# Kernel optimization log

Measured on AMD Instinct MI355X. Metric: run time of the kernel, lower is better.

Reference implementation:

```python
import jax, jax.numpy as jnp
import numpy as np

HEADS = 8
DIM_HEAD = 160
QUERY_DIM = 1280
INNER = HEADS * DIM_HEAD  # 1280
B, S = 2, 4096


def setup_inputs() -> dict:
    key = jax.random.key(0)
    ks = jax.random.split(key, 7)
    scale = 0.02
    return {
        "hidden_states": jax.random.normal(ks[0], (B, QUERY_DIM, 1, S), jnp.float32),
        "context": jax.random.normal(ks[1], (B, QUERY_DIM, 1, S), jnp.float32),
        "mask": jnp.zeros((B, S, 1, 1), jnp.float32),
        "Wq": jax.random.normal(ks[2], (INNER, QUERY_DIM), jnp.float32) * scale,
        "Wk": jax.random.normal(ks[3], (INNER, QUERY_DIM), jnp.float32) * scale,
        "Wv": jax.random.normal(ks[4], (INNER, QUERY_DIM), jnp.float32) * scale,
        "Wout": jax.random.normal(ks[5], (QUERY_DIM, INNER), jnp.float32) * scale,
        "bout": jnp.zeros((QUERY_DIM,), jnp.float32),
    }


def reference(hidden_states, context, mask, Wq, Wk, Wv, Wout, bout):
    # hidden_states/context: [B, C, 1, S]; 1x1 conv == channel-dim matmul.
    x = hidden_states[:, :, 0, :]  # [B, C, Sq]
    c = context[:, :, 0, :]        # [B, C, Sk]
    scale = DIM_HEAD ** (-0.5)

    q = jnp.einsum("oc,bcs->bos", Wq, x)  # [B, inner, Sq]
    k = jnp.einsum("oc,bcs->bos", Wk, c)  # [B, inner, Sk]
    v = jnp.einsum("oc,bcs->bos", Wv, c)  # [B, inner, Sk]

    bsz, _, sq = q.shape
    sk = k.shape[-1]
    qh = q.reshape(bsz, HEADS, DIM_HEAD, sq)
    kh = k.reshape(bsz, HEADS, DIM_HEAD, sk)
    vh = v.reshape(bsz, HEADS, DIM_HEAD, sk)

    # split_einsum: per-head q^T k * scale, mask added per kv position,
    # softmax over kv dim. Vectorized over heads here (same math).
    scores = jnp.einsum("bhdq,bhdk->bhqk", qh, kh) * scale  # [B,H,Sq,Sk]
    scores = scores + mask[:, 0:, 0, 0][:, None, None, :]   # mask over kv
    weights = jax.nn.softmax(scores, axis=-1)
    attn = jnp.einsum("bhqk,bhdk->bhdq", weights, vh)       # [B,H,Dh,Sq]
    attn = attn.reshape(bsz, INNER, sq)

    out = jnp.einsum("oc,bcs->bos", Wout, attn) + bout[None, :, None]
    return out[:, :, None, :]  # [B, C, 1, Sq]
```

## Files before the change

kernel.cpp:

```cpp
#include <hip/hip_runtime.h>
#include <hip/hip_bf16.h>
#include <math.h>

#define B_   2
#define S_   4096
#define H_   8
#define D_   160
#define QD_  1280
#define SCALE 0.07905694150420949f
#define LOG2E 1.4426950408889634f

typedef unsigned short ushort_t;
typedef __attribute__((ext_vector_type(8))) short short8;
typedef __attribute__((ext_vector_type(4))) float f32x4;

#define MFMA16(a, b, c) __builtin_amdgcn_mfma_f32_16x16x32_bf16(a, b, c, 0, 0, 0)

__device__ __forceinline__ ushort_t f2bf(float f) {
  unsigned u = __float_as_uint(f);
  u += 0x7fffu + ((u >> 16) & 1u);
  return (ushort_t)(u >> 16);
}
__device__ __forceinline__ ushort_t f2bf_fast(float f) {
  return (ushort_t)((__float_as_uint(f) + 0x8000u) >> 16);
}

__device__ __forceinline__ void gload_lds16(const ushort_t* g, ushort_t* l) {
  __builtin_amdgcn_global_load_lds(
      (const __attribute__((address_space(1))) unsigned int*)(g),
      (__attribute__((address_space(3))) unsigned int*)(l), 16, 0, 0);
}

template <int CTRL>
__device__ __forceinline__ float dpp_mov(float x) {
  return __int_as_float(
      __builtin_amdgcn_update_dpp(0, __float_as_int(x), CTRL, 0xF, 0xF, true));
}
__device__ __forceinline__ float row_sum16(float x) {
  x += dpp_mov<0xB1>(x);
  x += dpp_mov<0x4E>(x);
  x += dpp_mov<0x124>(x);
  x += dpp_mov<0x128>(x);
  return x;
}

__global__ __launch_bounds__(256) void transpose_cvt(
    const float* __restrict__ src, ushort_t* __restrict__ dst)
{
  const int b = blockIdx.z;
  const int s0 = blockIdx.x * 32;
  const int c0 = blockIdx.y * 32;
  __shared__ float T[32][33];
  const int t = threadIdx.x;
  const int sl = t & 31, cr = t >> 5;
#pragma unroll
  for (int i = 0; i < 4; ++i)
    T[cr + i * 8][sl] = src[((size_t)b * QD_ + c0 + cr + i * 8) * S_ + s0 + sl];
  __syncthreads();
  const int cl = (t & 7) * 4, sr = t >> 3;
  ushort4 v;
  v.x = f2bf(T[cl + 0][sr]);
  v.y = f2bf(T[cl + 1][sr]);
  v.z = f2bf(T[cl + 2][sr]);
  v.w = f2bf(T[cl + 3][sr]);
  *(ushort4*)(dst + ((size_t)b * S_ + s0 + sr) * QD_ + c0 + cl) = v;
}

__global__ __launch_bounds__(256) void cvt_w(
    const float* __restrict__ w0, const float* __restrict__ w1,
    const float* __restrict__ w2, const float* __restrict__ w3,
    ushort_t* __restrict__ o0, ushort_t* __restrict__ o1,
    ushort_t* __restrict__ o2, ushort_t* __restrict__ o3)
{
  const int which = blockIdx.y;
  const float* s = which == 0 ? w0 : which == 1 ? w1 : which == 2 ? w2 : w3;
  ushort_t* d    = which == 0 ? o0 : which == 1 ? o1 : which == 2 ? o2 : o3;
  const size_t i = ((size_t)blockIdx.x * 256 + threadIdx.x) * 4;
  const float4 f = *(const float4*)(s + i);
  ushort4 v;
  v.x = f2bf(f.x); v.y = f2bf(f.y); v.z = f2bf(f.z); v.w = f2bf(f.w);
  *(ushort4*)(d + i) = v;
}

#define GBM 128
#define GBN 128
#define GBK 32

__global__ __launch_bounds__(256) void gemm_mfma(
    const ushort_t* __restrict__ A, const ushort_t* __restrict__ B,
    void* __restrict__ Cp, const float* __restrict__ bias,
    int M, int N, int K, int mode,
    size_t strideA, size_t strideB, size_t strideC)
{
  const int bz = blockIdx.z;
  const int m0 = blockIdx.y * GBM;
  const int n0 = blockIdx.x * GBN;
  const ushort_t* __restrict__ Ab = A + (size_t)bz * strideA;
  const ushort_t* __restrict__ Bb = B + (size_t)bz * strideB;

  __shared__ ushort_t As[GBM * GBK];
  __shared__ ushort_t Bs[GBN * GBK];

  const int t = threadIdx.x;
  const int wid = t >> 6, lane = t & 63;
  const int l16 = lane & 15, quad = lane >> 4;
  const int wm = (wid >> 1) * 64, wn = (wid & 1) * 64;

  f32x4 acc[4][4];
#pragma unroll
  for (int i = 0; i < 4; ++i)
#pragma unroll
    for (int j = 0; j < 4; ++j) acc[i][j] = {0.f, 0.f, 0.f, 0.f};

  for (int k0 = 0; k0 < K; k0 += GBK) {
    __syncthreads();
#pragma unroll
    for (int i = 0; i < 2; ++i) {
      const int G = (i * 4 + wid) * 64 + lane;
      const int r = G >> 2, sl = G & 3;
      const int g = sl ^ (r & 3);
      gload_lds16(Ab + (size_t)(m0 + r) * K + k0 + g * 8, &As[(i * 4 + wid) * 512]);
      gload_lds16(Bb + (size_t)(n0 + r) * K + k0 + g * 8, &Bs[(i * 4 + wid) * 512]);
    }
    __syncthreads();

    short8 af[4], bfr[4];
#pragma unroll
    for (int mt = 0; mt < 4; ++mt) {
      const int r = wm + mt * 16 + l16;
      af[mt] = *(const short8*)&As[r * 32 + ((quad ^ (r & 3)) << 3)];
    }
#pragma unroll
    for (int nt = 0; nt < 4; ++nt) {
      const int r = wn + nt * 16 + l16;
      bfr[nt] = *(const short8*)&Bs[r * 32 + ((quad ^ (r & 3)) << 3)];
    }
#pragma unroll
    for (int mt = 0; mt < 4; ++mt)
#pragma unroll
      for (int nt = 0; nt < 4; ++nt)
        acc[mt][nt] = MFMA16(af[mt], bfr[nt], acc[mt][nt]);
  }

  if (mode == 0) {
    ushort_t* C = (ushort_t*)Cp + (size_t)bz * strideC;
#pragma unroll
    for (int mt = 0; mt < 4; ++mt)
#pragma unroll
      for (int r = 0; r < 4; ++r) {
        const int row = m0 + wm + mt * 16 + quad * 4 + r;
        ushort_t* cr = C + (size_t)row * N + n0 + wn + l16;
#pragma unroll
        for (int nt = 0; nt < 4; ++nt) cr[nt * 16] = f2bf_fast(acc[mt][nt][r]);
      }
  } else {
    float* C = (float*)Cp + (size_t)bz * strideC;
#pragma unroll
    for (int mt = 0; mt < 4; ++mt)
#pragma unroll
      for (int r = 0; r < 4; ++r) {
        const int row = m0 + wm + mt * 16 + quad * 4 + r;
        const float bv = bias[row];
        float* cr = C + (size_t)row * N + n0 + wn + l16;
#pragma unroll
        for (int nt = 0; nt < 4; ++nt) cr[nt * 16] = acc[mt][nt][r] + bv;
      }
  }
}

#define TQ 128
#define TK 64
#define KTSTR 168
#define VTSTR 72
#define PSTR  72

__global__ __launch_bounds__(256, 2) void flash_attn_mfma(
    const ushort_t* __restrict__ qws, const ushort_t* __restrict__ kws,
    const ushort_t* __restrict__ vws, const float* __restrict__ mask,
    ushort_t* __restrict__ attn_out)
{
  const int b  = blockIdx.z;
  const int h  = blockIdx.y;
  const int q0 = blockIdx.x * TQ;
  const int t  = threadIdx.x;
  const int wid  = t >> 6;
  const int lane = t & 63;
  const int l16  = lane & 15;
  const int quad = lane >> 4;

  __shared__ __align__(16) ushort_t smem[31744];
  ushort_t* Kt = smem;
  ushort_t* Vt = smem + 1344 * 8;
  ushort_t* Pp = smem + 2816 * 8;

  int goff[11];
#pragma unroll
  for (int jj = 0; jj < 11; ++jj) {
    const int j = jj * 4 + wid;
    const int slot = j * 64 + lane;
    int off;
    if (j < 21) {
      const int r = slot / 21, c = slot - r * 21;
      off = (c < 20) ? r * QD_ + c * 8 : 0;
    } else {
      const int vs = slot - 1344;
      const int r = vs / 9, c = vs - r * 9;
      off = (c < 8 && r < 160) ? r * S_ + c * 8 : 0;
    }
    goff[jj] = off;
  }

  short8 aq[2][5];
#pragma unroll
  for (int mt = 0; mt < 2; ++mt) {
    const ushort_t* qrow =
        qws + ((size_t)(b * S_ + q0 + wid * 32 + mt * 16 + l16)) * QD_ + h * D_;
#pragma unroll
    for (int dc = 0; dc < 5; ++dc)
      aq[mt][dc] = *(const short8*)(qrow + dc * 32 + quad * 8);
  }

  f32x4 Oa[2][10];
#pragma unroll
  for (int mt = 0; mt < 2; ++mt)
#pragma unroll
    for (int nt = 0; nt < 10; ++nt) Oa[mt][nt] = {0.f, 0.f, 0.f, 0.f};
  float lpart[2][4] = {{0.f, 0.f, 0.f, 0.f}, {0.f, 0.f, 0.f, 0.f}};
  const float SC2 = SCALE * LOG2E;

  for (int kp0 = 0; kp0 < S_; kp0 += TK) {
    const ushort_t* kg = kws + ((size_t)(b * S_ + kp0)) * QD_ + h * D_;
    const ushort_t* vg = vws + ((size_t)b * QD_ + h * D_) * S_ + kp0;
    __syncthreads();
#pragma unroll
    for (int jj = 0; jj < 11; ++jj) {
      const int j = jj * 4 + wid;
      const ushort_t* src = (j < 21) ? kg : vg;
      gload_lds16(src + goff[jj], &smem[(size_t)j * 512]);
    }
    __syncthreads();

    f32x4 s[2][4];
#pragma unroll
    for (int mt = 0; mt < 2; ++mt)
#pragma unroll
      for (int c = 0; c < 4; ++c) s[mt][c] = {0.f, 0.f, 0.f, 0.f};
#pragma unroll
    for (int dc = 0; dc < 5; ++dc) {
      short8 bb[4];
#pragma unroll
      for (int c = 0; c < 4; ++c)
        bb[c] = *(const short8*)&Kt[(c * 16 + l16) * KTSTR + dc * 32 + quad * 8];
#pragma unroll
      for (int mt = 0; mt < 2; ++mt)
#pragma unroll
        for (int c = 0; c < 4; ++c)
          s[mt][c] = MFMA16(aq[mt][dc], bb[c], s[mt][c]);
    }

    float mv[4];
#pragma unroll
    for (int c = 0; c < 4; ++c)
      mv[c] = mask[b * S_ + kp0 + c * 16 + l16] * LOG2E;

    ushort_t* pw = Pp + wid * (32 * PSTR);
#pragma unroll
    for (int mt = 0; mt < 2; ++mt)
#pragma unroll
      for (int r = 0; r < 4; ++r) {
        const float p0 = exp2f(s[mt][0][r] * SC2 + mv[0]);
        const float p1 = exp2f(s[mt][1][r] * SC2 + mv[1]);
        const float p2 = exp2f(s[mt][2][r] * SC2 + mv[2]);
        const float p3 = exp2f(s[mt][3][r] * SC2 + mv[3]);
        lpart[mt][r] += (p0 + p1) + (p2 + p3);
        ushort_t* prow = pw + (mt * 16 + quad * 4 + r) * PSTR;
        prow[l16]      = f2bf_fast(p0);
        prow[16 + l16] = f2bf_fast(p1);
        prow[32 + l16] = f2bf_fast(p2);
        prow[48 + l16] = f2bf_fast(p3);
      }

    short8 ap[2][2];
#pragma unroll
    for (int mt = 0; mt < 2; ++mt) {
#pragma unroll
      for (int ks = 0; ks < 2; ++ks)
        ap[mt][ks] = *(const short8*)
            &Pp[wid * (32 * PSTR) + (mt * 16 + l16) * PSTR + ks * 32 + quad * 8];
    }
#pragma unroll
    for (int nt = 0; nt < 10; ++nt) {
      const short8 bv0 = *(const short8*)&Vt[(nt * 16 + l16) * VTSTR + quad * 8];
      const short8 bv1 = *(const short8*)&Vt[(nt * 16 + l16) * VTSTR + 32 + quad * 8];
#pragma unroll
      for (int mt = 0; mt < 2; ++mt) {
        Oa[mt][nt] = MFMA16(ap[mt][0], bv0, Oa[mt][nt]);
        Oa[mt][nt] = MFMA16(ap[mt][1], bv1, Oa[mt][nt]);
      }
    }
  }

#pragma unroll
  for (int mt = 0; mt < 2; ++mt)
#pragma unroll
    for (int r = 0; r < 4; ++r) {
      const float l = row_sum16(lpart[mt][r]);
      const float inv = 1.f / l;
      const int qq = q0 + wid * 32 + mt * 16 + quad * 4 + r;
      ushort_t* orow = attn_out + ((size_t)(b * S_ + qq)) * QD_ + h * D_;
#pragma unroll
      for (int nt = 0; nt < 10; ++nt)
        orow[nt * 16 + l16] = f2bf_fast(Oa[mt][nt][r] * inv);
    }
}

extern "C" void kernel_launch(void* const* d_in, const int* in_sizes, int n_in,
                              void* d_out, int out_size, void* d_ws, size_t ws_size,
                              hipStream_t stream) {
  const float* x    = (const float*)d_in[0];
  const float* c    = (const float*)d_in[1];
  const float* mask = (const float*)d_in[2];
  const float* Wq   = (const float*)d_in[3];
  const float* Wk   = (const float*)d_in[4];
  const float* Wv   = (const float*)d_in[5];
  const float* Wout = (const float*)d_in[6];
  const float* bout = (const float*)d_in[7];
  float* out = (float*)d_out;

  const size_t PB   = (size_t)S_ * QD_;
  const size_t NELT = (size_t)B_ * PB;
  const size_t WN   = (size_t)QD_ * QD_;

  ushort_t* Xt    = (ushort_t*)d_ws;
  ushort_t* Ct    = Xt + NELT;
  ushort_t* Wqb   = Ct + NELT;
  ushort_t* Wkb   = Wqb + WN;
  ushort_t* Wvb   = Wkb + WN;
  ushort_t* Woutb = Wvb + WN;
  ushort_t* q_ws  = Woutb + WN;
  ushort_t* k_ws  = q_ws + NELT;
  ushort_t* v_ws  = k_ws + NELT;
  ushort_t* attn_ws = v_ws + NELT;

  const dim3 tgrid(S_ / 32, QD_ / 32, B_);
  transpose_cvt<<<tgrid, 256, 0, stream>>>(x, Xt);
  transpose_cvt<<<tgrid, 256, 0, stream>>>(c, Ct);
  cvt_w<<<dim3(WN / 1024, 4, 1), 256, 0, stream>>>(Wq, Wk, Wv, Wout,
                                                   Wqb, Wkb, Wvb, Woutb);

  const dim3 gq(QD_ / GBN, S_ / GBM, B_);
  gemm_mfma<<<gq, 256, 0, stream>>>(Xt, Wqb, q_ws, nullptr,
                                    S_, QD_, QD_, 0, PB, 0, PB);
  gemm_mfma<<<gq, 256, 0, stream>>>(Ct, Wkb, k_ws, nullptr,
                                    S_, QD_, QD_, 0, PB, 0, PB);
  const dim3 gv(S_ / GBN, QD_ / GBM, B_);
  gemm_mfma<<<gv, 256, 0, stream>>>(Wvb, Ct, v_ws, nullptr,
                                    QD_, S_, QD_, 0, 0, PB, PB);

  const dim3 agrid(S_ / TQ, H_, B_);
  flash_attn_mfma<<<agrid, 256, 0, stream>>>(q_ws, k_ws, v_ws, mask, attn_ws);

  gemm_mfma<<<gv, 256, 0, stream>>>(Woutb, attn_ws, out, bout,
                                    QD_, S_, QD_, 1, 0, PB, PB);
}
```

Baseline: 642.4 us.

## Overlap K/V tile loads with compute and swizzle P LDS layout

Restructures the attention inner loop so the next K tile is issued into LDS while the P·V MFMAs run, and the next V tile after the second barrier. The full syncthreads plus blocking load pairs are replaced with partial vmcnt waits and raw barriers. It also XOR-swizzles the P scratch layout to reduce LDS bank conflicts and raises wave priority around MFMA blocks. This risks subtle race or waitcnt miscounting issues since the vmcnt(5) depends on exact per-wave load counts.

```diff
diff --git a/kernel.cpp b/kernel.cpp
--- a/kernel.cpp
+++ b/kernel.cpp
@@ -210,6 +210,9 @@
     goff[jj] = off;
   }
 
+  const ushort_t* kg = kws + (size_t)b * S_ * QD_ + h * D_;
+  const ushort_t* vg = vws + ((size_t)b * QD_ + h * D_) * S_;
+
   short8 aq[2][5];
 #pragma unroll
   for (int mt = 0; mt < 2; ++mt) {
@@ -220,6 +223,17 @@
       aq[mt][dc] = *(const short8*)(qrow + dc * 32 + quad * 8);
   }
 
+#pragma unroll
+  for (int jj = 0; jj < 6; ++jj) {
+    const int j = jj * 4 + wid;
+    if (j < 21) gload_lds16(kg + goff[jj], &smem[(size_t)j * 512]);
+  }
+#pragma unroll
+  for (int jj = 5; jj < 11; ++jj) {
+    const int j = jj * 4 + wid;
+    if (j >= 21) gload_lds16(vg + goff[jj], &smem[(size_t)j * 512]);
+  }
+
   f32x4 Oa[2][10];
 #pragma unroll
   for (int mt = 0; mt < 2; ++mt)
@@ -228,23 +242,26 @@
   float lpart[2][4] = {{0.f, 0.f, 0.f, 0.f}, {0.f, 0.f, 0.f, 0.f}};
   const float SC2 = SCALE * LOG2E;
 
+  const int pswz = quad << 4;
+  const int prsw = (l16 >> 2) << 4;
+
   for (int kp0 = 0; kp0 < S_; kp0 += TK) {
-    const ushort_t* kg = kws + ((size_t)(b * S_ + kp0)) * QD_ + h * D_;
-    const ushort_t* vg = vws + ((size_t)b * QD_ + h * D_) * S_ + kp0;
-    __syncthreads();
-#pragma unroll
-    for (int jj = 0; jj < 11; ++jj) {
-      const int j = jj * 4 + wid;
-      const ushort_t* src = (j < 21) ? kg : vg;
-      gload_lds16(src + goff[jj], &smem[(size_t)j * 512]);
-    }
-    __syncthreads();
+    asm volatile("s_waitcnt vmcnt(5)" ::: "memory");
+    __builtin_amdgcn_sched_barrier(0);
+    __builtin_amdgcn_s_barrier();
+    __builtin_amdgcn_sched_barrier(0);
+
+    float mv[4];
+#pragma unroll
+    for (int c = 0; c < 4; ++c)
+      mv[c] = mask[b * S_ + kp0 + c * 16 + l16] * LOG2E;
 
     f32x4 s[2][4];
 #pragma unroll
     for (int mt = 0; mt < 2; ++mt)
 #pragma unroll
       for (int c = 0; c < 4; ++c) s[mt][c] = {0.f, 0.f, 0.f, 0.f};
+    __builtin_amdgcn_s_setprio(1);
 #pragma unroll
     for (int dc = 0; dc < 5; ++dc) {
       short8 bb[4];
@@ -257,11 +274,7 @@
         for (int c = 0; c < 4; ++c)
           s[mt][c] = MFMA16(aq[mt][dc], bb[c], s[mt][c]);
     }
-
-    float mv[4];
-#pragma unroll
-    for (int c = 0; c < 4; ++c)
-      mv[c] = mask[b * S_ + kp0 + c * 16 + l16] * LOG2E;
+    __builtin_amdgcn_s_setprio(0);
 
     ushort_t* pw = Pp + wid * (32 * PSTR);
 #pragma unroll
@@ -274,10 +287,10 @@
         const float p3 = exp2f(s[mt][3][r] * SC2 + mv[3]);
         lpart[mt][r] += (p0 + p1) + (p2 + p3);
         ushort_t* prow = pw + (mt * 16 + quad * 4 + r) * PSTR;
-        prow[l16]      = f2bf_fast(p0);
-        prow[16 + l16] = f2bf_fast(p1);
-        prow[32 + l16] = f2bf_fast(p2);
-        prow[48 + l16] = f2bf_fast(p3);
+        prow[(pswz ^  0) + l16] = f2bf_fast(p0);
+        prow[(pswz ^ 16) + l16] = f2bf_fast(p1);
+        prow[(pswz ^ 32) + l16] = f2bf_fast(p2);
+        prow[(pswz ^ 48) + l16] = f2bf_fast(p3);
       }
 
     short8 ap[2][2];
@@ -286,8 +299,24 @@
 #pragma unroll
       for (int ks = 0; ks < 2; ++ks)
         ap[mt][ks] = *(const short8*)
-            &Pp[wid * (32 * PSTR) + (mt * 16 + l16) * PSTR + ks * 32 + quad * 8];
-    }
+            &Pp[wid * (32 * PSTR) + (mt * 16 + l16) * PSTR +
+                ((ks * 32 + quad * 8) ^ prsw)];
+    }
+
+    __syncthreads();
+
+    const int kn = kp0 + TK;
+    if (kn < S_) {
+      const ushort_t* kgn = kg + (size_t)kn * QD_;
+#pragma unroll
+      for (int jj = 0; jj < 6; ++jj) {
+        const int j = jj * 4 + wid;
+        if (j < 21) gload_lds16(kgn + goff[jj], &smem[(size_t)j * 512]);
+      }
+      __builtin_amdgcn_sched_barrier(0);
+    }
+
+    __builtin_amdgcn_s_setprio(1);
 #pragma unroll
     for (int nt = 0; nt < 10; ++nt) {
       const short8 bv0 = *(const short8*)&Vt[(nt * 16 + l16) * VTSTR + quad * 8];
@@ -296,6 +325,20 @@
       for (int mt = 0; mt < 2; ++mt) {
         Oa[mt][nt] = MFMA16(ap[mt][0], bv0, Oa[mt][nt]);
         Oa[mt][nt] = MFMA16(ap[mt][1], bv1, Oa[mt][nt]);
+      }
+    }
+    __builtin_amdgcn_s_setprio(0);
+
+    __builtin_amdgcn_sched_barrier(0);
+    __builtin_amdgcn_s_barrier();
+    __builtin_amdgcn_sched_barrier(0);
+
+    if (kn < S_) {
+      const ushort_t* vgn = vg + kn;
+#pragma unroll
+      for (int jj = 5; jj < 11; ++jj) {
+        const int j = jj * 4 + wid;
+        if (j >= 21) gload_lds16(vgn + goff[jj], &smem[(size_t)j * 512]);
       }
     }
   }
```

Result: faster. 622.5 us (-3.1%).
